# Kernel tuning notes

Measured on AMD Instinct MI355X. Metric: run time of the kernel, lower is better.

The kernel has to match this reference:

```python
import jax, jax.numpy as jnp
import numpy as np

B_SZ, L, D, N = 4, 2048, 768, 16


def setup_inputs() -> dict:
    key = jax.random.key(0)
    ks = jax.random.split(key, 8)
    x = jax.random.normal(ks[0], (B_SZ, L, D), dtype=jnp.float32)
    # A_log initialized as log(arange(1..N)) repeated over d, as in the module
    A_log = jnp.log(jnp.broadcast_to(jnp.arange(1, N + 1, dtype=jnp.float32), (D, N)))
    # s_b_c: Linear(D, 2N)
    W_bc = jax.random.normal(ks[1], (2 * N, D), dtype=jnp.float32) / jnp.sqrt(D)
    b_bc = jnp.zeros((2 * N,), dtype=jnp.float32)
    # s_1: Linear(D, 1)
    W_1 = jax.random.normal(ks[2], (1, D), dtype=jnp.float32) / jnp.sqrt(D)
    b_1 = jnp.zeros((1,), dtype=jnp.float32)
    # s_delta: Linear(1, D)
    W_d = jax.random.normal(ks[3], (D, 1), dtype=jnp.float32)
    b_d = jnp.zeros((D,), dtype=jnp.float32)
    return {"x": x, "A_log": A_log, "W_bc": W_bc, "b_bc": b_bc,
            "W_1": W_1, "b_1": b_1, "W_d": W_d, "b_d": b_d}


def reference(x, A_log, W_bc, b_bc, W_1, b_1, W_d, b_d):
    b, l, d = x.shape
    n = A_log.shape[1]
    A = -jnp.exp(A_log)                                   # (d, n)
    BandC = x @ W_bc.T + b_bc                             # (b, l, 2n)
    Bm, Cm = BandC[..., :n], BandC[..., n:]               # (b, l, n) each
    # delta = softplus(s_delta(s_1(x)))  -> (b, l, d)
    s1 = x @ W_1.T + b_1                                  # (b, l, 1)
    delta = jax.nn.softplus(s1 @ W_d.T + b_d)             # (b, l, d)
    deltaA = jnp.exp(jnp.einsum('bld,dn->bldn', delta, A))        # (b, l, d, n)
    deltaB_u = jnp.einsum('bld,bln,bld->bldn', delta, Bm, x)      # (b, l, d, n)

    # sequential selective-scan over time with lax.scan
    dA_t = jnp.moveaxis(deltaA, 1, 0)      # (l, b, d, n)
    dBu_t = jnp.moveaxis(deltaB_u, 1, 0)   # (l, b, d, n)
    C_t = jnp.moveaxis(Cm, 1, 0)           # (l, b, n)

    def step(h, inp):
        dA_i, dBu_i, c_i = inp
        h = dA_i * h + dBu_i               # (b, d, n)
        y = jnp.einsum('bdn,bn->bd', h, c_i)
        return h, y

    h0 = jnp.zeros((b, d, n), dtype=x.dtype)
    _, ys = jax.lax.scan(step, h0, (dA_t, dBu_t, C_t))
    return jnp.moveaxis(ys, 0, 1)          # (b, l, d)
```

## Files before the change

### kernel.cpp

```cpp
#include <hip/hip_runtime.h>

#define L_SEQ 2048
#define D_DIM 768
#define N_ST 16
#define NB 4
#define NJ 33
#define BCS 48
#define NROWS (NB * L_SEQ)
#define PROJ_ELEMS (NROWS * NJ)
#define DN (D_DIM * N_ST)

#define DSPLIT 8
#define DSEG (D_DIM / DSPLIT)
#define DK 32
#define NCHUNK (DSEG / DK)
#define RB 128
#define XST 132
#define WST 64

typedef float v2f __attribute__((ext_vector_type(2)));

__device__ __forceinline__ float fast_exp2(float x) {
#if __has_builtin(__builtin_amdgcn_exp2f)
  return __builtin_amdgcn_exp2f(x);
#else
  return __expf(x * 0.69314718055994531f);
#endif
}

__device__ __forceinline__ float softplus_f(float v) {
  float e = fast_exp2(v * 1.44269504088896f);
  float l = __log2f(1.0f + e) * 0.69314718055994531f;
  return (v > 15.0f) ? v : l;
}

__device__ __forceinline__ void pow_tree2(float e1, v2f pw2[8]) {
  float e2s = e1 * e1;
  float e4s = e2s * e2s;
  float e8s = e4s * e4s;
  v2f s2 = {e2s, e2s}, s4 = {e4s, e4s}, s8 = {e8s, e8s};
  pw2[0] = (v2f){e1, e2s};
  pw2[1] = pw2[0] * s2;
  pw2[2] = pw2[0] * s4;
  pw2[3] = pw2[1] * s4;
  pw2[4] = pw2[0] * s8;
  pw2[5] = pw2[1] * s8;
  pw2[6] = pw2[2] * s8;
  pw2[7] = pw2[3] * s8;
}

__global__ __launch_bounds__(256) void k_proj_gemm(
    const float* __restrict__ x, const float* __restrict__ W_bc,
    const float* __restrict__ W_1, float* __restrict__ PBC) {
  __shared__ float xs_t[DK * XST];
  __shared__ float ws_t[DK * WST];

  const int ds  = blockIdx.x % DSPLIT;
  const int rb0 = (blockIdx.x / DSPLIT) * RB;
  const int dbase = ds * DSEG;
  const int tid = threadIdx.x;
  const int rg = tid & 31;
  const int jg = tid >> 5;

  float acc[4][5];
#pragma unroll
  for (int i = 0; i < 4; ++i)
#pragma unroll
    for (int k = 0; k < 5; ++k) acc[i][k] = 0.0f;

  const int lrow = tid >> 1;
  const int lhalf = (tid & 1) * 16;
  const float* xg_row = x + (size_t)(rb0 + lrow) * D_DIM + dbase + lhalf;

  for (int ch = 0; ch < NCHUNK; ++ch) {
    const int dc = dbase + ch * DK;
    float4 xv[4];
#pragma unroll
    for (int q = 0; q < 4; ++q)
      xv[q] = *(const float4*)(xg_row + ch * DK + q * 4);
    float wv[8];
    int widx[8];
#pragma unroll
    for (int u = 0; u < 8; ++u) {
      int idx = tid + u * 256;
      int dk = idx >> 6, slot = idx & 63;
      int wjg = slot >> 3, wk = slot & 7;
      int j = wjg + 8 * wk;
      float v = 0.0f;
      if (wk < 5) {
        if (j < 32)       v = W_bc[(size_t)j * D_DIM + dc + dk];
        else if (j == 32) v = W_1[dc + dk];
      }
      wv[u] = v; widx[u] = dk * WST + slot;
    }
    __syncthreads();
#pragma unroll
    for (int q = 0; q < 4; ++q) {
      xs_t[(lhalf + q * 4 + 0) * XST + lrow] = xv[q].x;
      xs_t[(lhalf + q * 4 + 1) * XST + lrow] = xv[q].y;
      xs_t[(lhalf + q * 4 + 2) * XST + lrow] = xv[q].z;
      xs_t[(lhalf + q * 4 + 3) * XST + lrow] = xv[q].w;
    }
#pragma unroll
    for (int u = 0; u < 8; ++u) ws_t[widx[u]] = wv[u];
    __syncthreads();
#pragma unroll 8
    for (int dk = 0; dk < DK; ++dk) {
      float4 xr = *(const float4*)&xs_t[dk * XST + rg * 4];
      float4 wr = *(const float4*)&ws_t[dk * WST + jg * 8];
      float w4  = ws_t[dk * WST + jg * 8 + 4];
      float xa[4] = {xr.x, xr.y, xr.z, xr.w};
      float wa[5] = {wr.x, wr.y, wr.z, wr.w, w4};
#pragma unroll
      for (int i = 0; i < 4; ++i)
#pragma unroll
        for (int k = 0; k < 5; ++k)
          acc[i][k] = fmaf(xa[i], wa[k], acc[i][k]);
    }
  }

  float* pb = PBC + (size_t)ds * PROJ_ELEMS;
#pragma unroll
  for (int i = 0; i < 4; ++i) {
    int row = rb0 + rg * 4 + i;
#pragma unroll
    for (int k = 0; k < 5; ++k) {
      int j = jg + 8 * k;
      if (k < 4 || jg == 0) pb[(size_t)row * NJ + j] = acc[i][k];
    }
  }
}

__global__ __launch_bounds__(256) void k_proj_reduce(
    const float* __restrict__ PBC, const float* __restrict__ b_bc,
    const float* __restrict__ b_1, float* __restrict__ BC48) {
  const int idx = blockIdx.x * 256 + threadIdx.x;
  const int row = idx / NJ;
  const int j = idx - row * NJ;
  float s = 0.0f;
#pragma unroll
  for (int k = 0; k < DSPLIT; ++k) s += PBC[(size_t)k * PROJ_ELEMS + idx];
  s += (j < 32) ? b_bc[j] : b_1[0];
  BC48[(size_t)row * BCS + j] = s;
}

template <int LC>
__global__ __launch_bounds__(256, 6) void k_scan1(
    const float* __restrict__ x, const float* __restrict__ A_log,
    const float* __restrict__ W_d, const float* __restrict__ b_d,
    const float* __restrict__ BC48, float* __restrict__ DS,
    float* __restrict__ H, int NC) {
  const int cb = blockIdx.x % 3;
  const int c  = (blockIdx.x / 3) % NC;
  const int b  = blockIdx.x / (3 * NC);
  const int d  = cb * 256 + threadIdx.x;

  const float wd = W_d[d], bd = b_d[d];
  float Aln[N_ST];
  {
    const float4* al4 = (const float4*)(A_log + (size_t)d * N_ST);
#pragma unroll
    for (int q = 0; q < 4; ++q) {
      float4 v = al4[q];
      Aln[4*q+0] = -__expf(v.x) * 1.44269504088896f;
      Aln[4*q+1] = -__expf(v.y) * 1.44269504088896f;
      Aln[4*q+2] = -__expf(v.z) * 1.44269504088896f;
      Aln[4*q+3] = -__expf(v.w) * 1.44269504088896f;
    }
  }
  bool geom = true;
#pragma unroll
  for (int n = 1; n < N_ST; ++n) {
    float ref = (float)(n + 1) * Aln[0];
    geom = geom && (fabsf(Aln[n] - ref) <= 1e-4f * fabsf(ref) + 1e-12f);
  }
  const float a0 = Aln[0];

  v2f h2[8];
#pragma unroll
  for (int k = 0; k < 8; ++k) h2[k] = (v2f){0.0f, 0.0f};
  float dsum = 0.0f;

  const int l0 = c * LC;
  const float* bc = BC48 + (size_t)(b * L_SEQ + l0) * BCS;
  const float* xp = x + (size_t)(b * L_SEQ + l0) * D_DIM + d;

  if (geom) {
#pragma unroll 8
    for (int l = 0; l < LC; ++l) {
      const float* r = bc + l * BCS;
      float4 B0 = *(const float4*)(r + 0);
      float4 B1 = *(const float4*)(r + 4);
      float4 B2 = *(const float4*)(r + 8);
      float4 B3 = *(const float4*)(r + 12);
      float s1 = r[32];
      float delta = softplus_f(fmaf(s1, wd, bd));
      float xv = xp[(size_t)l * D_DIM];
      float f = delta * xv;
      dsum += delta;
      v2f pw2[8];
      pow_tree2(fast_exp2(a0 * delta), pw2);
      v2f f2 = {f, f};
      h2[0] = pw2[0] * h2[0] + f2 * (v2f){B0.x, B0.y};
      h2[1] = pw2[1] * h2[1] + f2 * (v2f){B0.z, B0.w};
      h2[2] = pw2[2] * h2[2] + f2 * (v2f){B1.x, B1.y};
      h2[3] = pw2[3] * h2[3] + f2 * (v2f){B1.z, B1.w};
      h2[4] = pw2[4] * h2[4] + f2 * (v2f){B2.x, B2.y};
      h2[5] = pw2[5] * h2[5] + f2 * (v2f){B2.z, B2.w};
      h2[6] = pw2[6] * h2[6] + f2 * (v2f){B3.x, B3.y};
      h2[7] = pw2[7] * h2[7] + f2 * (v2f){B3.z, B3.w};
    }
  } else {
#pragma unroll 4
    for (int l = 0; l < LC; ++l) {
      const float* r = bc + l * BCS;
      float s1 = r[32];
      float delta = softplus_f(fmaf(s1, wd, bd));
      float f = delta * xp[(size_t)l * D_DIM];
      dsum += delta;
#pragma unroll
      for (int k = 0; k < 8; ++k) {
        h2[k].x = fmaf(fast_exp2(delta * Aln[2*k]),   h2[k].x, f * r[2*k]);
        h2[k].y = fmaf(fast_exp2(delta * Aln[2*k+1]), h2[k].y, f * r[2*k+1]);
      }
    }
  }

  DS[((size_t)b * NC + c) * D_DIM + d] = dsum;
  size_t base = ((size_t)(b * NC + c) * D_DIM + d) * N_ST;
  float4* H4 = (float4*)(H + base);
#pragma unroll
  for (int q = 0; q < 4; ++q)
    H4[q] = make_float4(h2[2*q].x, h2[2*q].y, h2[2*q+1].x, h2[2*q+1].y);
}

__global__ __launch_bounds__(256) void k_combine(
    const float* __restrict__ A_log, const float* __restrict__ DS,
    float* __restrict__ H, int NC) {
  const int b  = blockIdx.x / 48;
  const int tl = (blockIdx.x % 48) * 256 + threadIdx.x;
  const int d = tl >> 4, n = tl & 15;
  const float Aln1 = -__expf(A_log[d * N_ST + n]) * 1.44269504088896f;
  const float* dsp = DS + (size_t)b * NC * D_DIM + d;
  float* Hp = H + (size_t)b * NC * DN + tl;

  float h = 0.0f;
  float pds[8], ph[8];
#pragma unroll
  for (int k = 0; k < 8; ++k) {
    pds[k] = dsp[(size_t)k * D_DIM];
    ph[k]  = Hp[(size_t)k * DN];
  }
  for (int g = 0; g < NC; g += 8) {
    float nds[8], nh[8];
    if (g + 8 < NC) {
#pragma unroll
      for (int k = 0; k < 8; ++k) {
        nds[k] = dsp[(size_t)(g + 8 + k) * D_DIM];
        nh[k]  = Hp[(size_t)(g + 8 + k) * DN];
      }
    }
#pragma unroll
    for (int k = 0; k < 8; ++k) {
      float p = fast_exp2(Aln1 * pds[k]);
      Hp[(size_t)(g + k) * DN] = h;
      h = fmaf(p, h, ph[k]);
    }
#pragma unroll
    for (int k = 0; k < 8; ++k) { pds[k] = nds[k]; ph[k] = nh[k]; }
  }
}

template <int LC>
__global__ __launch_bounds__(256, 6) void k_scan2(
    const float* __restrict__ x, const float* __restrict__ A_log,
    const float* __restrict__ W_d, const float* __restrict__ b_d,
    const float* __restrict__ BC48, const float* __restrict__ HIN,
    float* __restrict__ out, int NC) {
  const int cb = blockIdx.x % 3;
  const int c  = (blockIdx.x / 3) % NC;
  const int b  = blockIdx.x / (3 * NC);
  const int d  = cb * 256 + threadIdx.x;

  const float wd = W_d[d], bd = b_d[d];
  float Aln[N_ST];
  {
    const float4* al4 = (const float4*)(A_log + (size_t)d * N_ST);
#pragma unroll
    for (int q = 0; q < 4; ++q) {
      float4 v = al4[q];
      Aln[4*q+0] = -__expf(v.x) * 1.44269504088896f;
      Aln[4*q+1] = -__expf(v.y) * 1.44269504088896f;
      Aln[4*q+2] = -__expf(v.z) * 1.44269504088896f;
      Aln[4*q+3] = -__expf(v.w) * 1.44269504088896f;
    }
  }
  bool geom = true;
#pragma unroll
  for (int n = 1; n < N_ST; ++n) {
    float ref = (float)(n + 1) * Aln[0];
    geom = geom && (fabsf(Aln[n] - ref) <= 1e-4f * fabsf(ref) + 1e-12f);
  }
  const float a0 = Aln[0];

  v2f h2[8];
  {
    size_t base = ((size_t)(b * NC + c) * D_DIM + d) * N_ST;
    const float4* HIN4 = (const float4*)(HIN + base);
#pragma unroll
    for (int q = 0; q < 4; ++q) {
      float4 v = HIN4[q];
      h2[2*q]   = (v2f){v.x, v.y};
      h2[2*q+1] = (v2f){v.z, v.w};
    }
  }

  const int l0 = c * LC;
  const float* bc = BC48 + (size_t)(b * L_SEQ + l0) * BCS;
  const float* xp = x + (size_t)(b * L_SEQ + l0) * D_DIM + d;
  float* op = out + (size_t)(b * L_SEQ + l0) * D_DIM + d;

  if (geom) {
#pragma unroll 8
    for (int l = 0; l < LC; ++l) {
      const float* r = bc + l * BCS;
      float4 B0 = *(const float4*)(r + 0);
      float4 B1 = *(const float4*)(r + 4);
      float4 B2 = *(const float4*)(r + 8);
      float4 B3 = *(const float4*)(r + 12);
      float4 C0 = *(const float4*)(r + 16);
      float4 C1 = *(const float4*)(r + 20);
      float4 C2 = *(const float4*)(r + 24);
      float4 C3 = *(const float4*)(r + 28);
      float s1 = r[32];
      float delta = softplus_f(fmaf(s1, wd, bd));
      float xv = xp[(size_t)l * D_DIM];
      float f = delta * xv;
      v2f pw2[8];
      pow_tree2(fast_exp2(a0 * delta), pw2);
      v2f f2 = {f, f};
      v2f y2 = {0.0f, 0.0f};
      h2[0] = pw2[0] * h2[0] + f2 * (v2f){B0.x, B0.y};  y2 += h2[0] * (v2f){C0.x, C0.y};
      h2[1] = pw2[1] * h2[1] + f2 * (v2f){B0.z, B0.w};  y2 += h2[1] * (v2f){C0.z, C0.w};
      h2[2] = pw2[2] * h2[2] + f2 * (v2f){B1.x, B1.y};  y2 += h2[2] * (v2f){C1.x, C1.y};
      h2[3] = pw2[3] * h2[3] + f2 * (v2f){B1.z, B1.w};  y2 += h2[3] * (v2f){C1.z, C1.w};
      h2[4] = pw2[4] * h2[4] + f2 * (v2f){B2.x, B2.y};  y2 += h2[4] * (v2f){C2.x, C2.y};
      h2[5] = pw2[5] * h2[5] + f2 * (v2f){B2.z, B2.w};  y2 += h2[5] * (v2f){C2.z, C2.w};
      h2[6] = pw2[6] * h2[6] + f2 * (v2f){B3.x, B3.y};  y2 += h2[6] * (v2f){C3.x, C3.y};
      h2[7] = pw2[7] * h2[7] + f2 * (v2f){B3.z, B3.w};  y2 += h2[7] * (v2f){C3.z, C3.w};
      op[(size_t)l * D_DIM] = y2.x + y2.y;
    }
  } else {
#pragma unroll 4
    for (int l = 0; l < LC; ++l) {
      const float* r = bc + l * BCS;
      float s1 = r[32];
      float delta = softplus_f(fmaf(s1, wd, bd));
      float f = delta * xp[(size_t)l * D_DIM];
      float y = 0.0f;
#pragma unroll
      for (int k = 0; k < 8; ++k) {
        h2[k].x = fmaf(fast_exp2(delta * Aln[2*k]),   h2[k].x, f * r[2*k]);
        h2[k].y = fmaf(fast_exp2(delta * Aln[2*k+1]), h2[k].y, f * r[2*k+1]);
        y = fmaf(h2[k].x, r[16 + 2*k], y);
        y = fmaf(h2[k].y, r[16 + 2*k + 1], y);
      }
      op[(size_t)l * D_DIM] = y;
    }
  }
}

extern "C" void kernel_launch(void* const* d_in, const int* in_sizes, int n_in,
                              void* d_out, int out_size, void* d_ws, size_t ws_size,
                              hipStream_t stream) {
  const float* x     = (const float*)d_in[0];
  const float* A_log = (const float*)d_in[1];
  const float* W_bc  = (const float*)d_in[2];
  const float* b_bc  = (const float*)d_in[3];
  const float* W_1   = (const float*)d_in[4];
  const float* b_1   = (const float*)d_in[5];
  const float* W_d   = (const float*)d_in[6];
  const float* b_d   = (const float*)d_in[7];
  float* out = (float*)d_out;
  float* ws  = (float*)d_ws;

  int NC = 128;
  {
    size_t need = ((size_t)NROWS * BCS + 8ull * PROJ_ELEMS +
                   (3072ull + 49152ull) * 128) * 4ull;
    if (ws_size < need) NC = 64;
  }

  float* BC48 = ws;
  float* PBC  = ws + (size_t)NROWS * BCS;
  float* DSb  = PBC + (size_t)DSPLIT * PROJ_ELEMS;
  float* H    = DSb + (size_t)3072 * NC;

  k_proj_gemm<<<(NROWS / RB) * DSPLIT, 256, 0, stream>>>(x, W_bc, W_1, PBC);
  k_proj_reduce<<<(PROJ_ELEMS + 255) / 256, 256, 0, stream>>>(PBC, b_bc, b_1, BC48);

  const int gs = 3 * NB * NC;
  if (NC == 128) {
    k_scan1<16><<<gs, 256, 0, stream>>>(x, A_log, W_d, b_d, BC48, DSb, H, NC);
    k_combine<<<192, 256, 0, stream>>>(A_log, DSb, H, NC);
    k_scan2<16><<<gs, 256, 0, stream>>>(x, A_log, W_d, b_d, BC48, H, out, NC);
  } else {
    k_scan1<32><<<gs, 256, 0, stream>>>(x, A_log, W_d, b_d, BC48, DSb, H, NC);
    k_combine<<<192, 256, 0, stream>>>(A_log, DSb, H, NC);
    k_scan2<32><<<gs, 256, 0, stream>>>(x, A_log, W_d, b_d, BC48, H, out, NC);
  }
}
```

Measured before the change: 152.1 us.

## Parallelize chunk-combine scan across chunks with two-level block scan

Replaces the serial per-(d,n) combine over all chunks with a two-level scan: 8 warps each aggregate a contiguous group of chunks, share (P,H) aggregates in LDS, then each warp computes its prefix and writes carry-in states. The grid grows from 192 to 1536 blocks, turning a long serial latency chain into more parallel work. It costs some redundant prefix work and 32-wide coalesced accesses instead of 256-wide.

```diff
diff --git a/kernel.cpp b/kernel.cpp
--- a/kernel.cpp
+++ b/kernel.cpp
@@ -234,40 +234,51 @@
     H4[q] = make_float4(h2[2*q].x, h2[2*q].y, h2[2*q+1].x, h2[2*q+1].y);
 }
 
-__global__ __launch_bounds__(256) void k_combine(
+template <int SC>
+__global__ __launch_bounds__(256) void k_combine_par(
     const float* __restrict__ A_log, const float* __restrict__ DS,
     float* __restrict__ H, int NC) {
-  const int b  = blockIdx.x / 48;
-  const int tl = (blockIdx.x % 48) * 256 + threadIdx.x;
-  const int d = tl >> 4, n = tl & 15;
-  const float Aln1 = -__expf(A_log[d * N_ST + n]) * 1.44269504088896f;
+  __shared__ float Pl[8 * 33];
+  __shared__ float Hl[8 * 33];
+  const int b    = blockIdx.x / 384;
+  const int dn0  = (blockIdx.x % 384) * 32;
+  const int lane = threadIdx.x & 31;
+  const int j    = threadIdx.x >> 5;
+  const int dn   = dn0 + lane;
+  const int d    = dn >> 4;
+
+  const float Aln1 = -__expf(A_log[dn]) * 1.44269504088896f;
+
   const float* dsp = DS + (size_t)b * NC * D_DIM + d;
-  float* Hp = H + (size_t)b * NC * DN + tl;
+  float* Hp = H + (size_t)b * NC * DN + dn;
+
+  float p[SC], ph[SC];
+#pragma unroll
+  for (int k = 0; k < SC; ++k) {
+    const int c = j * SC + k;
+    p[k]  = fast_exp2(Aln1 * dsp[(size_t)c * D_DIM]);
+    ph[k] = Hp[(size_t)c * DN];
+  }
+
+  float Pagg = 1.0f, Hagg = 0.0f;
+#pragma unroll
+  for (int k = 0; k < SC; ++k) {
+    Hagg = fmaf(p[k], Hagg, ph[k]);
+    Pagg *= p[k];
+  }
+
+  Pl[j * 33 + lane] = Pagg;
+  Hl[j * 33 + lane] = Hagg;
+  __syncthreads();
 
   float h = 0.0f;
-  float pds[8], ph[8];
-#pragma unroll
-  for (int k = 0; k < 8; ++k) {
-    pds[k] = dsp[(size_t)k * D_DIM];
-    ph[k]  = Hp[(size_t)k * DN];
-  }
-  for (int g = 0; g < NC; g += 8) {
-    float nds[8], nh[8];
-    if (g + 8 < NC) {
-#pragma unroll
-      for (int k = 0; k < 8; ++k) {
-        nds[k] = dsp[(size_t)(g + 8 + k) * D_DIM];
-        nh[k]  = Hp[(size_t)(g + 8 + k) * DN];
-      }
-    }
-#pragma unroll
-    for (int k = 0; k < 8; ++k) {
-      float p = fast_exp2(Aln1 * pds[k]);
-      Hp[(size_t)(g + k) * DN] = h;
-      h = fmaf(p, h, ph[k]);
-    }
-#pragma unroll
-    for (int k = 0; k < 8; ++k) { pds[k] = nds[k]; ph[k] = nh[k]; }
+  for (int j2 = 0; j2 < j; ++j2)
+    h = fmaf(Pl[j2 * 33 + lane], h, Hl[j2 * 33 + lane]);
+
+#pragma unroll
+  for (int k = 0; k < SC; ++k) {
+    Hp[(size_t)(j * SC + k) * DN] = h;
+    h = fmaf(p[k], h, ph[k]);
   }
 }
 
@@ -402,11 +413,11 @@
   const int gs = 3 * NB * NC;
   if (NC == 128) {
     k_scan1<16><<<gs, 256, 0, stream>>>(x, A_log, W_d, b_d, BC48, DSb, H, NC);
-    k_combine<<<192, 256, 0, stream>>>(A_log, DSb, H, NC);
+    k_combine_par<16><<<NB * 384, 256, 0, stream>>>(A_log, DSb, H, NC);
     k_scan2<16><<<gs, 256, 0, stream>>>(x, A_log, W_d, b_d, BC48, H, out, NC);
   } else {
     k_scan1<32><<<gs, 256, 0, stream>>>(x, A_log, W_d, b_d, BC48, DSb, H, NC);
-    k_combine<<<192, 256, 0, stream>>>(A_log, DSb, H, NC);
+    k_combine_par<8><<<NB * 384, 256, 0, stream>>>(A_log, DSb, H, NC);
     k_scan2<32><<<gs, 256, 0, stream>>>(x, A_log, W_d, b_d, BC48, H, out, NC);
   }
 }
```

After: 151.2 us. About the same (-0.6%).
